# Optimization experiments

Measured on AMD Instinct MI355X. Metric: run time of the kernel, lower is better.

Reference implementation:

```python
import jax, jax.numpy as jnp
import numpy as np

B, O, N, D = 32, 2, 4096, 128


def setup_inputs() -> dict:
    key = jax.random.key(0)
    ks = jax.random.split(key, 5)
    stdv = 1.0 / float(np.sqrt(D))
    x = jax.random.normal(ks[0], (B, O, N, D), dtype=jnp.float32)
    last_nodes = jax.random.randint(ks[1], (B, O), 0, N, dtype=jnp.int32)
    # torch Linear weight is [out,in]; y = x @ W.T + b. Store Wu as [O, out, in].
    Wu = jax.random.uniform(ks[2], (O, D, D), jnp.float32, -stdv, stdv)
    bu = jnp.zeros((O, D), jnp.float32)  # reset_parameters sets biases to 0
    Wv = jax.random.uniform(ks[3], (O, D, D), jnp.float32, -stdv, stdv)
    We = jax.random.uniform(ks[4], (O, D), jnp.float32, -stdv, stdv)  # fc_e weight row [1,D] -> [D]
    return {"x": x, "Wu": Wu, "bu": bu, "Wv": Wv, "We": We, "last_nodes": last_nodes}


def reference(x, Wu, bu, Wv, We, last_nodes):
    # x: [B, O, N, D]; last_nodes: [B, O] indices into N
    Bz, Oz, Nz, Dz = x.shape
    # gather last node per (batch, order): [B, O, D]
    x_last = x[jnp.arange(Bz)[:, None], jnp.arange(Oz)[None, :], last_nodes]
    # per-order-i projection of the FULL x (each order attends over all O*N nodes)
    # xu: [B, I, O, N, D] where I indexes the attention head (order loop index)
    xu = jnp.einsum('bond,ied->bione', x, Wu) + bu[None, :, None, None, :]
    # xv: [B, I, D]
    xv = jnp.einsum('bid,ied->bie', x_last, Wv)
    s = jax.nn.sigmoid(xu + xv[:, :, None, None, :])
    # scalar score per node: [B, I, O, N] -> [B, I, O*N]
    e = jnp.einsum('bione,ie->bion', s, We).reshape(Bz, Oz, Oz * Nz)
    alpha = jax.nn.softmax(e, axis=-1)  # stable softmax over node axis
    x_all = x.reshape(Bz, Oz * Nz, Dz)
    # weighted-sum pooling: [B, I, D]
    out = jnp.einsum('bim,bmd->bid', alpha, x_all)
    return out
```

## Files before the change

### kernel.cpp

```cpp
#include <hip/hip_runtime.h>
#include <hip/hip_bf16.h>
#include <math.h>

#define B_ 32
#define O_ 2
#define N_ 4096
#define D_ 128
#define M_ (O_*N_)
#define MC 512

typedef __bf16 bf16x8 __attribute__((ext_vector_type(8)));
typedef float  f32x4  __attribute__((ext_vector_type(4)));

static __device__ __forceinline__ unsigned short f2bf(float f) {
    unsigned int u = __float_as_uint(f);
    u += 0x7fffu + ((u >> 16) & 1u);
    return (unsigned short)(u >> 16);
}

__global__ __launch_bounds__(256) void k_prep(const float* __restrict__ Wu,
        unsigned short* __restrict__ wub) {
    int idx = blockIdx.x*256 + threadIdx.x;
    wub[idx] = f2bf(Wu[idx]);
}

__global__ __launch_bounds__(128) void k_cvec(const float* __restrict__ x,
        const float* __restrict__ Wv, const float* __restrict__ bu,
        const int* __restrict__ last, float* __restrict__ cvec)
{
    int bi = blockIdx.x;
    int b = bi >> 1, i = bi & 1;
    int e = threadIdx.x;
    __shared__ float xl[D_];
    int ln = last[bi];
    const float* xrow = x + (((size_t)b*O_ + i)*N_ + ln)*D_;
    xl[e] = xrow[e];
    __syncthreads();
    const float* wv = Wv + ((size_t)i*D_ + e)*D_;
    float acc = bu[i*D_ + e];
    #pragma unroll 8
    for (int d = 0; d < D_; ++d) acc += xl[d]*wv[d];
    cvec[bi*D_ + e] = acc;
}

__global__ __launch_bounds__(256, 2) void k_logits_mfma(
        const float* __restrict__ x, const unsigned short* __restrict__ wub,
        const float* __restrict__ cvec, const float* __restrict__ We,
        float* __restrict__ logits)
{
    __shared__ uint4 ldsbuf[4096];
    unsigned char* lds = (unsigned char*)ldsbuf;
    unsigned char* xsb = lds;
    unsigned char* wsb = lds + 32768;
    float* red = (float*)lds;

    int blk  = blockIdx.x;
    int tile = blk & 31;
    int o    = (blk >> 5) & 1;
    int b    = blk >> 6;
    int n0   = tile * 128;

    int t = threadIdx.x;
    int l = t & 63;
    int w = t >> 6;
    int wr = w >> 1, wc = w & 1;
    int l15 = l & 15, lq = l >> 4;

    const float* xbase = x + (((size_t)b*O_ + o)*N_ + n0)*D_;

    #pragma unroll
    for (int it = 0; it < 16; ++it) {
        int idx = it*256 + t;
        int row = idx >> 5;
        int c   = idx & 31;
        float4 v = *(const float4*)(xbase + row*D_ + c*4);
        ushort4 h;
        h.x = f2bf(v.x); h.y = f2bf(v.y); h.z = f2bf(v.z); h.w = f2bf(v.w);
        int ks = c >> 3, cc = c & 7;
        int off = (ks*64 + (cc&3)*16 + (cc>>2)*8) ^ ((row & 15) << 4);
        *(ushort4*)(xsb + row*256 + off) = h;
    }
    __syncthreads();

    bf16x8 Af[4][4];
    #pragma unroll
    for (int ks = 0; ks < 4; ++ks) {
        #pragma unroll
        for (int m = 0; m < 4; ++m) {
            int row = wr*64 + m*16 + l15;
            int off = (ks*64 + lq*16) ^ ((row & 15) << 4);
            uint4 u = *(const uint4*)(xsb + row*256 + off);
            Af[ks][m] = __builtin_bit_cast(bf16x8, u);
        }
    }
    __syncthreads();

    f32x4 zero = {0.f, 0.f, 0.f, 0.f};

    for (int i = 0; i < O_; ++i) {
        const unsigned short* wsrc = wub + i*D_*D_;
        #pragma unroll
        for (int it = 0; it < 16; ++it) {
            int idx = it*256 + t;
            int e = idx >> 5;
            int c = idx & 31;
            int ks = c >> 3, cc = c & 7;
            int off = (ks*64 + (cc&3)*16 + (cc>>2)*8) ^ ((e & 15) << 4);
            *(ushort4*)(wsb + e*256 + off) = *(const ushort4*)(wsrc + e*D_ + c*4);
        }
        __syncthreads();

        f32x4 acc[4][4];
        #pragma unroll
        for (int m = 0; m < 4; ++m)
            #pragma unroll
            for (int n = 0; n < 4; ++n)
                acc[m][n] = zero;

        #pragma unroll
        for (int ks = 0; ks < 4; ++ks) {
            bf16x8 Bf[4];
            #pragma unroll
            for (int n = 0; n < 4; ++n) {
                int e = wc*64 + n*16 + l15;
                int off = (ks*64 + lq*16) ^ ((e & 15) << 4);
                uint4 u = *(const uint4*)(wsb + e*256 + off);
                Bf[n] = __builtin_bit_cast(bf16x8, u);
            }
            #pragma unroll
            for (int m = 0; m < 4; ++m)
                #pragma unroll
                for (int n = 0; n < 4; ++n)
                    acc[m][n] = __builtin_amdgcn_mfma_f32_16x16x32_bf16(
                        Af[ks][m], Bf[n], acc[m][n], 0, 0, 0);
        }
        __syncthreads();

        int bi = b*O_ + i;
        float cv[4], wev[4];
        #pragma unroll
        for (int n = 0; n < 4; ++n) {
            int e = wc*64 + n*16 + l15;
            cv[n]  = cvec[bi*D_ + e];
            wev[n] = We[i*D_ + e];
        }
        #pragma unroll
        for (int m = 0; m < 4; ++m) {
            float pv[4] = {0.f, 0.f, 0.f, 0.f};
            #pragma unroll
            for (int n = 0; n < 4; ++n) {
                #pragma unroll
                for (int r = 0; r < 4; ++r) {
                    float z = acc[m][n][r] + cv[n];
                    float s = __builtin_amdgcn_rcpf(1.f + __expf(-z));
                    pv[r] += s * wev[n];
                }
            }
            #pragma unroll
            for (int off = 1; off < 16; off <<= 1) {
                #pragma unroll
                for (int r = 0; r < 4; ++r)
                    pv[r] += __shfl_xor(pv[r], off);
            }
            if (l15 == 0) {
                int rb = wr*64 + m*16 + lq*4;
                #pragma unroll
                for (int r = 0; r < 4; ++r)
                    red[wc*128 + rb + r] = pv[r];
            }
        }
        __syncthreads();
        if (t < 128)
            logits[(size_t)bi*M_ + o*N_ + n0 + t] = red[t] + red[128 + t];
        __syncthreads();
    }
}

__global__ __launch_bounds__(256) void k_stats(const float* __restrict__ logits,
        float* __restrict__ stats)
{
    int bi = blockIdx.x, t = threadIdx.x;
    const float* lg = logits + (size_t)bi*M_;
    __shared__ float red[4];
    __shared__ float red2[4];

    float mx = -1e30f;
    for (int m = t; m < M_; m += 256) mx = fmaxf(mx, lg[m]);
    #pragma unroll
    for (int off = 32; off >= 1; off >>= 1) mx = fmaxf(mx, __shfl_xor(mx, off));
    if ((t & 63) == 0) red[t >> 6] = mx;
    __syncthreads();
    mx = fmaxf(fmaxf(red[0], red[1]), fmaxf(red[2], red[3]));

    float sm = 0.f;
    for (int m = t; m < M_; m += 256) sm += __expf(lg[m] - mx);
    #pragma unroll
    for (int off = 32; off >= 1; off >>= 1) sm += __shfl_xor(sm, off);
    if ((t & 63) == 0) red2[t >> 6] = sm;
    __syncthreads();
    if (t == 0) {
        sm = red2[0] + red2[1] + red2[2] + red2[3];
        stats[bi*2]     = mx;
        stats[bi*2 + 1] = 1.f/sm;
    }
}

__global__ __launch_bounds__(128) void k_wsum(const float* __restrict__ logits,
        const float* __restrict__ stats, const float* __restrict__ x,
        float* __restrict__ part)
{
    int blk = blockIdx.x;
    int chunk = blk & 15;
    int bi = blk >> 4;
    int b = bi >> 1;
    int t = threadIdx.x;
    float mx  = stats[bi*2];
    float inv = stats[bi*2 + 1];
    const float* lg = logits + (size_t)bi*M_;
    float acc = 0.f;
    int m0 = chunk*MC;
    #pragma unroll 8
    for (int mm = 0; mm < MC; ++mm) {
        int m = m0 + mm;
        float wgt = __expf(lg[m] - mx)*inv;
        const float* xr = x + ((size_t)b*M_ + m)*D_;
        acc += wgt * xr[t];
    }
    part[(size_t)blk*D_ + t] = acc;
}

__global__ __launch_bounds__(128) void k_red(const float* __restrict__ part,
        float* __restrict__ out)
{
    int bi = blockIdx.x, t = threadIdx.x;
    float s = 0.f;
    #pragma unroll
    for (int c = 0; c < 16; ++c) s += part[(size_t)(bi*16 + c)*D_ + t];
    out[bi*D_ + t] = s;
}

extern "C" void kernel_launch(void* const* d_in, const int* in_sizes, int n_in,
                              void* d_out, int out_size, void* d_ws, size_t ws_size,
                              hipStream_t stream) {
    const float* x    = (const float*)d_in[0];
    const float* Wu   = (const float*)d_in[1];
    const float* bu   = (const float*)d_in[2];
    const float* Wv   = (const float*)d_in[3];
    const float* We   = (const float*)d_in[4];
    const int*   last = (const int*)d_in[5];
    float* out = (float*)d_out;

    float* ws      = (float*)d_ws;
    float* logits  = ws;
    float* cvec    = logits + (size_t)B_*O_*M_;
    float* stats   = cvec + B_*O_*D_;
    float* part    = stats + B_*O_*2;
    unsigned short* wub = (unsigned short*)(part + (size_t)B_*O_*16*D_);

    k_prep       <<<128, 256, 0, stream>>>(Wu, wub);
    k_cvec       <<<B_*O_, 128, 0, stream>>>(x, Wv, bu, last, cvec);
    k_logits_mfma<<<B_*O_*(N_/128), 256, 0, stream>>>(x, wub, cvec, We, logits);
    k_stats      <<<B_*O_, 256, 0, stream>>>(logits, stats);
    k_wsum       <<<B_*O_*(M_/MC), 128, 0, stream>>>(logits, stats, x, part);
    k_red        <<<B_*O_, 128, 0, stream>>>(part, out);
}
```

Before: 100.4 us.

## Fuse softmax stats into logits kernel, read pre-permuted weights from global, vectorize wsum

The logits kernel now emits per-64-node partial max and sum-exp, which k_wsum merges online, so the separate k_stats pass over the logits is gone. Wu is converted to bf16 in a pre-permuted fragment layout, and B fragments are loaded straight from global/L2 instead of being staged in LDS. This removes two barriers per order and cuts LDS use, which may raise occupancy. k_wsum now precomputes the weights in shared memory and reads x as float4 across 8 row-slices per block. The cost is redundant global weight loads per wave.

```diff
diff --git a/kernel.cpp b/kernel.cpp
--- a/kernel.cpp
+++ b/kernel.cpp
@@ -7,7 +7,6 @@
 #define N_ 4096
 #define D_ 128
 #define M_ (O_*N_)
-#define MC 512
 
 typedef __bf16 bf16x8 __attribute__((ext_vector_type(8)));
 typedef float  f32x4  __attribute__((ext_vector_type(4)));
@@ -19,9 +18,15 @@
 }
 
 __global__ __launch_bounds__(256) void k_prep(const float* __restrict__ Wu,
-        unsigned short* __restrict__ wub) {
+        unsigned short* __restrict__ wup) {
     int idx = blockIdx.x*256 + threadIdx.x;
-    wub[idx] = f2bf(Wu[idx]);
+    int i = idx >> 12, e = (idx >> 5) & 127, c = idx & 31;
+    int ks = c >> 3, cc = c & 7;
+    float4 v = *(const float4*)(Wu + ((size_t)(i*D_ + e))*D_ + c*4);
+    ushort4 h;
+    h.x = f2bf(v.x); h.y = f2bf(v.y); h.z = f2bf(v.z); h.w = f2bf(v.w);
+    int pos = ks*32 + (cc&3)*8 + (cc>>2)*4;
+    *(ushort4*)(wup + ((size_t)(i*D_ + e))*D_ + pos) = h;
 }
 
 __global__ __launch_bounds__(128) void k_cvec(const float* __restrict__ x,
@@ -44,15 +49,12 @@
 }
 
 __global__ __launch_bounds__(256, 2) void k_logits_mfma(
-        const float* __restrict__ x, const unsigned short* __restrict__ wub,
+        const float* __restrict__ x, const unsigned short* __restrict__ wup,
         const float* __restrict__ cvec, const float* __restrict__ We,
-        float* __restrict__ logits)
-{
-    __shared__ uint4 ldsbuf[4096];
-    unsigned char* lds = (unsigned char*)ldsbuf;
-    unsigned char* xsb = lds;
-    unsigned char* wsb = lds + 32768;
-    float* red = (float*)lds;
+        float* __restrict__ logits, float* __restrict__ tstats)
+{
+    __shared__ unsigned char xsb[32768];
+    __shared__ float red[256];
 
     int blk  = blockIdx.x;
     int tile = blk & 31;
@@ -93,22 +95,12 @@
             Af[ks][m] = __builtin_bit_cast(bf16x8, u);
         }
     }
-    __syncthreads();
 
     f32x4 zero = {0.f, 0.f, 0.f, 0.f};
 
+    #pragma unroll
     for (int i = 0; i < O_; ++i) {
-        const unsigned short* wsrc = wub + i*D_*D_;
-        #pragma unroll
-        for (int it = 0; it < 16; ++it) {
-            int idx = it*256 + t;
-            int e = idx >> 5;
-            int c = idx & 31;
-            int ks = c >> 3, cc = c & 7;
-            int off = (ks*64 + (cc&3)*16 + (cc>>2)*8) ^ ((e & 15) << 4);
-            *(ushort4*)(wsb + e*256 + off) = *(const ushort4*)(wsrc + e*D_ + c*4);
-        }
-        __syncthreads();
+        const unsigned short* wb = wup + (size_t)i*D_*D_;
 
         f32x4 acc[4][4];
         #pragma unroll
@@ -123,8 +115,7 @@
             #pragma unroll
             for (int n = 0; n < 4; ++n) {
                 int e = wc*64 + n*16 + l15;
-                int off = (ks*64 + lq*16) ^ ((e & 15) << 4);
-                uint4 u = *(const uint4*)(wsb + e*256 + off);
+                uint4 u = *(const uint4*)(wb + e*D_ + ks*32 + lq*8);
                 Bf[n] = __builtin_bit_cast(bf16x8, u);
             }
             #pragma unroll
@@ -134,7 +125,6 @@
                     acc[m][n] = __builtin_amdgcn_mfma_f32_16x16x32_bf16(
                         Af[ks][m], Bf[n], acc[m][n], 0, 0, 0);
         }
-        __syncthreads();
 
         int bi = b*O_ + i;
         float cv[4], wev[4];
@@ -170,43 +160,28 @@
             }
         }
         __syncthreads();
-        if (t < 128)
-            logits[(size_t)bi*M_ + o*N_ + n0 + t] = red[t] + red[128 + t];
+        if (t < 128) {
+            float lg = red[t] + red[128 + t];
+            logits[(size_t)bi*M_ + o*N_ + n0 + t] = lg;
+            float mx = lg;
+            #pragma unroll
+            for (int off = 1; off < 64; off <<= 1) mx = fmaxf(mx, __shfl_xor(mx, off));
+            float sm = __expf(lg - mx);
+            #pragma unroll
+            for (int off = 1; off < 64; off <<= 1) sm += __shfl_xor(sm, off);
+            if ((t & 63) == 0) {
+                int g = o*32 + tile;
+                int j = g*2 + (t >> 6);
+                tstats[(size_t)bi*256 + j*2]     = mx;
+                tstats[(size_t)bi*256 + j*2 + 1] = sm;
+            }
+        }
         __syncthreads();
     }
 }
 
-__global__ __launch_bounds__(256) void k_stats(const float* __restrict__ logits,
-        float* __restrict__ stats)
-{
-    int bi = blockIdx.x, t = threadIdx.x;
-    const float* lg = logits + (size_t)bi*M_;
-    __shared__ float red[4];
-    __shared__ float red2[4];
-
-    float mx = -1e30f;
-    for (int m = t; m < M_; m += 256) mx = fmaxf(mx, lg[m]);
-    #pragma unroll
-    for (int off = 32; off >= 1; off >>= 1) mx = fmaxf(mx, __shfl_xor(mx, off));
-    if ((t & 63) == 0) red[t >> 6] = mx;
-    __syncthreads();
-    mx = fmaxf(fmaxf(red[0], red[1]), fmaxf(red[2], red[3]));
-
-    float sm = 0.f;
-    for (int m = t; m < M_; m += 256) sm += __expf(lg[m] - mx);
-    #pragma unroll
-    for (int off = 32; off >= 1; off >>= 1) sm += __shfl_xor(sm, off);
-    if ((t & 63) == 0) red2[t >> 6] = sm;
-    __syncthreads();
-    if (t == 0) {
-        sm = red2[0] + red2[1] + red2[2] + red2[3];
-        stats[bi*2]     = mx;
-        stats[bi*2 + 1] = 1.f/sm;
-    }
-}
-
-__global__ __launch_bounds__(128) void k_wsum(const float* __restrict__ logits,
-        const float* __restrict__ stats, const float* __restrict__ x,
+__global__ __launch_bounds__(256) void k_wsum(const float* __restrict__ logits,
+        const float* __restrict__ tstats, const float* __restrict__ x,
         float* __restrict__ part)
 {
     int blk = blockIdx.x;
@@ -214,19 +189,53 @@
     int bi = blk >> 4;
     int b = bi >> 1;
     int t = threadIdx.x;
-    float mx  = stats[bi*2];
-    float inv = stats[bi*2 + 1];
-    const float* lg = logits + (size_t)bi*M_;
-    float acc = 0.f;
-    int m0 = chunk*MC;
+    int lane = t & 63, w = t >> 6;
+
+    __shared__ float wbuf[512];
+    __shared__ float pacc[8][128];
+    __shared__ float sred[8];
+
+    const float* ts = tstats + (size_t)bi*256;
+    float my_m = (t < 128) ? ts[t*2]     : -1e30f;
+    float my_s = (t < 128) ? ts[t*2 + 1] : 0.f;
+    float m = my_m;
+    #pragma unroll
+    for (int off = 1; off < 64; off <<= 1) m = fmaxf(m, __shfl_xor(m, off));
+    if (lane == 0) sred[w] = m;
+    __syncthreads();
+    m = fmaxf(fmaxf(sred[0], sred[1]), fmaxf(sred[2], sred[3]));
+    float c = (t < 128) ? my_s*__expf(my_m - m) : 0.f;
+    #pragma unroll
+    for (int off = 1; off < 64; off <<= 1) c += __shfl_xor(c, off);
+    if (lane == 0) sred[4 + w] = c;
+    __syncthreads();
+    float inv = 1.f/(sred[4] + sred[5] + sred[6] + sred[7]);
+
+    int m0 = chunk*512;
+    const float* lg = logits + (size_t)bi*M_ + m0;
+    wbuf[t]       = __expf(lg[t]       - m)*inv;
+    wbuf[t + 256] = __expf(lg[t + 256] - m)*inv;
+    __syncthreads();
+
+    int d4 = t & 31, s = t >> 5;
+    f32x4 a = {0.f, 0.f, 0.f, 0.f};
+    const float* xb = x + ((size_t)b*M_ + m0)*D_ + d4*4;
     #pragma unroll 8
-    for (int mm = 0; mm < MC; ++mm) {
-        int m = m0 + mm;
-        float wgt = __expf(lg[m] - mx)*inv;
-        const float* xr = x + ((size_t)b*M_ + m)*D_;
-        acc += wgt * xr[t];
-    }
-    part[(size_t)blk*D_ + t] = acc;
+    for (int r = 0; r < 64; ++r) {
+        int row = s*64 + r;
+        float wgt = wbuf[row];
+        f32x4 xv = *(const f32x4*)(xb + (size_t)row*D_);
+        a += wgt*xv;
+    }
+    #pragma unroll
+    for (int j = 0; j < 4; ++j) pacc[s][d4*4 + j] = a[j];
+    __syncthreads();
+    if (t < 128) {
+        float acc = 0.f;
+        #pragma unroll
+        for (int st = 0; st < 8; ++st) acc += pacc[st][t];
+        part[(size_t)blk*D_ + t] = acc;
+    }
 }
 
 __global__ __launch_bounds__(128) void k_red(const float* __restrict__ part,
@@ -253,14 +262,13 @@
     float* ws      = (float*)d_ws;
     float* logits  = ws;
     float* cvec    = logits + (size_t)B_*O_*M_;
-    float* stats   = cvec + B_*O_*D_;
-    float* part    = stats + B_*O_*2;
-    unsigned short* wub = (unsigned short*)(part + (size_t)B_*O_*16*D_);
-
-    k_prep       <<<128, 256, 0, stream>>>(Wu, wub);
+    float* tstats  = cvec + B_*O_*D_;
+    float* part    = tstats + (size_t)B_*O_*256;
+    unsigned short* wup = (unsigned short*)(part + (size_t)B_*O_*16*D_);
+
+    k_prep       <<<32, 256, 0, stream>>>(Wu, wup);
     k_cvec       <<<B_*O_, 128, 0, stream>>>(x, Wv, bu, last, cvec);
-    k_logits_mfma<<<B_*O_*(N_/128), 256, 0, stream>>>(x, wub, cvec, We, logits);
-    k_stats      <<<B_*O_, 256, 0, stream>>>(logits, stats);
-    k_wsum       <<<B_*O_*(M_/MC), 128, 0, stream>>>(logits, stats, x, part);
+    k_logits_mfma<<<B_*O_*(N_/128), 256, 0, stream>>>(x, wup, cvec, We, logits, tstats);
+    k_wsum       <<<B_*O_*(M_/512), 256, 0, stream>>>(logits, tstats, x, part);
     k_red        <<<B_*O_, 128, 0, stream>>>(part, out);
 }
```

Measured after the change: 102.9 us. 2.5% more time.
